# Optimization experiments

Hardware: AMD Instinct MI355X
Metric: run time of the kernel (lower is better)

## Reference

```python
import jax, jax.numpy as jnp
import numpy as np

N = 50000          # nodes
E = 800000         # directed edges (avg degree 16)
IN_F = 1433        # Cora num_features
N_CLS = 7          # Cora num_classes
HEADS = 8
HID = 32
NEG_SLOPE = 0.2    # PyG GATConv default negative_slope


def gat_conv(x, src, dst, W, a_src, a_dst, bias, heads, out_ch):
    """PyG GATConv (concat=True, add_self_loops=True, eval mode)."""
    n = x.shape[0]
    h = (x @ W).reshape(n, heads, out_ch)            # [N, H, C]
    # add self loops (PyG default)
    loop = jnp.arange(n, dtype=src.dtype)
    src = jnp.concatenate([src, loop])
    dst = jnp.concatenate([dst, loop])
    # attention logits per edge: a_src . h_src + a_dst . h_dst
    alpha_src = (h * a_src).sum(-1)                  # [N, H]
    alpha_dst = (h * a_dst).sum(-1)                  # [N, H]
    e = jax.nn.leaky_relu(alpha_src[src] + alpha_dst[dst], NEG_SLOPE)  # [E+N, H]
    # segment softmax over incoming edges of each destination node
    m = jax.ops.segment_max(e, dst, num_segments=n)  # [N, H]
    p = jnp.exp(e - m[dst])
    denom = jax.ops.segment_sum(p, dst, num_segments=n)
    alpha = p / denom[dst]                           # [E+N, H]
    # attention-weighted scatter-aggregate of source features
    out = jax.ops.segment_sum(h[src] * alpha[:, :, None], dst, num_segments=n)  # [N, H, C]
    return out.reshape(n, heads * out_ch) + bias


def setup_inputs() -> dict:
    key = jax.random.key(0)
    ks = jax.random.split(key, 12)
    s = 0.05
    x = jax.random.normal(ks[0], (N, IN_F), dtype=jnp.float32)
    edge_index = jax.random.randint(ks[1], (2, E), 0, N, dtype=jnp.int32)
    W1 = jax.random.normal(ks[2], (IN_F, HEADS * HID), dtype=jnp.float32) * s
    att_src1 = jax.random.normal(ks[3], (HEADS, HID), dtype=jnp.float32) * s
    att_dst1 = jax.random.normal(ks[4], (HEADS, HID), dtype=jnp.float32) * s
    bias1 = jnp.zeros((HEADS * HID,), dtype=jnp.float32)
    W2 = jax.random.normal(ks[5], (HEADS * HID, HEADS * N_CLS), dtype=jnp.float32) * s
    att_src2 = jax.random.normal(ks[6], (HEADS, N_CLS), dtype=jnp.float32) * s
    att_dst2 = jax.random.normal(ks[7], (HEADS, N_CLS), dtype=jnp.float32) * s
    bias2 = jnp.zeros((HEADS * N_CLS,), dtype=jnp.float32)
    return {
        "x": x, "edge_index": edge_index,
        "W1": W1, "att_src1": att_src1, "att_dst1": att_dst1, "bias1": bias1,
        "W2": W2, "att_src2": att_src2, "att_dst2": att_dst2, "bias2": bias2,
    }


def reference(x, edge_index, W1, att_src1, att_dst1, bias1,
              W2, att_src2, att_dst2, bias2):
    src, dst = edge_index[0], edge_index[1]
    # dropout (p=0.6) is identity in eval mode
    h = gat_conv(x, src, dst, W1, att_src1, att_dst1, bias1, HEADS, HID)
    h = jax.nn.elu(h)
    out = gat_conv(h, src, dst, W2, att_src2, att_dst2, bias2, HEADS, N_CLS)
    return out  # [N, HEADS * N_CLS]
```

## Files before the change

### kernel.cpp

```cpp
#include <hip/hip_runtime.h>
#include <math.h>

typedef short s16x8 __attribute__((ext_vector_type(8)));
typedef float f32x4 __attribute__((ext_vector_type(4)));

#define SLOPE 0.2f
#define K1 1433
#define KP 1440
#define NKB 45

static __device__ __forceinline__ float leaky(float x) {
  return x > 0.f ? x : SLOPE * x;
}

static __device__ __forceinline__ unsigned short f2bf(float f) {
  unsigned u = __builtin_bit_cast(unsigned, f);
  u += 0x7FFFu + ((u >> 16) & 1u);
  return (unsigned short)(u >> 16);
}
static __device__ __forceinline__ float bf2f(unsigned short h) {
  unsigned u = ((unsigned)h) << 16;
  return __builtin_bit_cast(float, u);
}

__global__ void w1t_kernel(const float* __restrict__ W1,
                           unsigned short* __restrict__ w1f) {
  int tid = blockIdx.x * 256 + threadIdx.x;
  if (tid >= NKB * 2 * 16 * 64) return;
  int l = tid & 63;
  int chunk = tid >> 6;
  int ntg = chunk & 15;
  int hl = (chunk >> 4) & 1;
  int kb = chunk >> 5;
  int n = ntg * 16 + (l & 15);
  int kbase = kb * 32 + (l >> 4) * 8;
  unsigned short o[8];
#pragma unroll
  for (int e = 0; e < 8; ++e) {
    int k = kbase + e;
    float v = (k < K1) ? W1[(long)k * 256 + n] : 0.f;
    unsigned short h = f2bf(v);
    o[e] = hl ? f2bf(v - bf2f(h)) : h;
  }
  *(ulonglong2*)(w1f + (long)tid * 8) = *(ulonglong2*)o;
}

__global__ __launch_bounds__(256) void gemm1_mfma_kernel(
    const float* __restrict__ A, const unsigned short* __restrict__ w1f,
    float* __restrict__ C, int M) {
  __shared__ unsigned short As[8 * 2 * 64 * 8];
  __shared__ unsigned short Bs[8 * 2 * 64 * 8];
  const int t = threadIdx.x;
  const int w = t >> 6, l = t & 63;
  const int wm = w >> 1, wn = w & 1;
  const int row0 = blockIdx.x * 128;
  const int nblk = blockIdx.y;

  f32x4 acc[4][4];
#pragma unroll
  for (int mt = 0; mt < 4; ++mt)
#pragma unroll
    for (int nt = 0; nt < 4; ++nt)
#pragma unroll
      for (int r = 0; r < 4; ++r) acc[mt][nt][r] = 0.f;

  const int sr = t >> 1;
  const int sk = (t & 1) * 16;
  const int smt = sr >> 4;
  const int slr = sr & 15;

  for (int kb = 0; kb < NKB; ++kb) {
    const int k0 = kb * 32;
#pragma unroll
    for (int q = 0; q < 4; ++q) {
      int c = w * 4 + q;
      int nt = c >> 1, hl = c & 1;
      const unsigned short* gsrc =
          w1f + ((((long)kb * 2 + hl) * 16 + nblk * 8 + nt) * 64 + l) * 8;
      unsigned short* ldst = &Bs[(nt * 2 + hl) * 512];
      __builtin_amdgcn_global_load_lds(
          (const __attribute__((address_space(1))) unsigned int*)gsrc,
          (__attribute__((address_space(3))) unsigned int*)ldst, 16, 0, 0);
    }
    {
      int grow = row0 + sr;
      float v[16];
      if (grow < M) {
        const float* ap = A + (long)grow * K1;
#pragma unroll
        for (int i = 0; i < 16; ++i) {
          int gk = k0 + sk + i;
          v[i] = (gk < K1) ? ap[gk] : 0.f;
        }
      } else {
#pragma unroll
        for (int i = 0; i < 16; ++i) v[i] = 0.f;
      }
#pragma unroll
      for (int g = 0; g < 2; ++g) {
        unsigned short hv[8], lv[8];
#pragma unroll
        for (int e = 0; e < 8; ++e) {
          float f = v[g * 8 + e];
          unsigned short h = f2bf(f);
          hv[e] = h;
          lv[e] = f2bf(f - bf2f(h));
        }
        int lane_dst = slr + 16 * (sk / 8 + g);
        *(ulonglong2*)&As[((smt * 2 + 0) * 64 + lane_dst) * 8] = *(ulonglong2*)hv;
        *(ulonglong2*)&As[((smt * 2 + 1) * 64 + lane_dst) * 8] = *(ulonglong2*)lv;
      }
    }
    __syncthreads();
    {
      s16x8 bh[4], bl[4];
#pragma unroll
      for (int nt = 0; nt < 4; ++nt) {
        int ng = wn * 4 + nt;
        bh[nt] = *(const s16x8*)&Bs[(ng * 2 + 0) * 512 + l * 8];
        bl[nt] = *(const s16x8*)&Bs[(ng * 2 + 1) * 512 + l * 8];
      }
#pragma unroll
      for (int mt = 0; mt < 4; ++mt) {
        int mg = wm * 4 + mt;
        s16x8 ah = *(const s16x8*)&As[(mg * 2 + 0) * 512 + l * 8];
        s16x8 al = *(const s16x8*)&As[(mg * 2 + 1) * 512 + l * 8];
#pragma unroll
        for (int nt = 0; nt < 4; ++nt) {
          acc[mt][nt] = __builtin_amdgcn_mfma_f32_16x16x32_bf16(
              ah, bh[nt], acc[mt][nt], 0, 0, 0);
          acc[mt][nt] = __builtin_amdgcn_mfma_f32_16x16x32_bf16(
              ah, bl[nt], acc[mt][nt], 0, 0, 0);
          acc[mt][nt] = __builtin_amdgcn_mfma_f32_16x16x32_bf16(
              al, bh[nt], acc[mt][nt], 0, 0, 0);
        }
      }
    }
    __syncthreads();
  }
  const int crow4 = (l >> 4) * 4;
  const int ccol = l & 15;
#pragma unroll
  for (int mt = 0; mt < 4; ++mt) {
#pragma unroll
    for (int r = 0; r < 4; ++r) {
      int grow = row0 + wm * 64 + mt * 16 + crow4 + r;
      if (grow < M) {
#pragma unroll
        for (int nt = 0; nt < 4; ++nt) {
          int gcol = nblk * 128 + wn * 64 + nt * 16 + ccol;
          C[(long)grow * 256 + gcol] = acc[mt][nt][r];
        }
      }
    }
  }
}

__global__ void alpha1_kernel(const float* __restrict__ h1,
    const float* __restrict__ a_src, const float* __restrict__ a_dst,
    float* __restrict__ as_o, float* __restrict__ ad_o, int N) {
  int i = blockIdx.x * blockDim.x + threadIdx.x;
  if (i >= N * 8) return;
  int h = i & 7;
  const float* hp = h1 + (long)(i >> 3) * 256 + h * 32;
  const float* sp = a_src + h * 32;
  const float* dp = a_dst + h * 32;
  float s1 = 0.f, s2 = 0.f;
#pragma unroll
  for (int c = 0; c < 32; c += 4) {
    float4 v = *(const float4*)(hp + c);
    float4 ws = *(const float4*)(sp + c);
    float4 wd = *(const float4*)(dp + c);
    s1 += v.x * ws.x + v.y * ws.y + v.z * ws.z + v.w * ws.w;
    s2 += v.x * wd.x + v.y * wd.y + v.z * wd.z + v.w * wd.w;
  }
  as_o[i] = s1;
  ad_o[i] = s2;
}

__global__ void hist_kernel(const int* __restrict__ dst, int* __restrict__ cnt,
                            int E, int N) {
  int e = blockIdx.x * blockDim.x + threadIdx.x;
  if (e >= E + N) return;
  int d = (e < E) ? dst[e] : (e - E);
  atomicAdd(&cnt[d], 1);
}

__global__ __launch_bounds__(1024) void scan_kernel(
    const int* __restrict__ cnt, int* __restrict__ rowptr,
    int* __restrict__ cursor, int N) {
  __shared__ int part[1024];
  const int tid = threadIdx.x;
  const int chunk = (N + 1023) / 1024;
  const int base = tid * chunk;
  const int lim = min(base + chunk, N);
  int sum = 0;
  for (int i = base; i < lim; ++i) sum += cnt[i];
  part[tid] = sum;
  __syncthreads();
  for (int off = 1; off < 1024; off <<= 1) {
    int v = (tid >= off) ? part[tid - off] : 0;
    __syncthreads();
    part[tid] += v;
    __syncthreads();
  }
  int run = (tid == 0) ? 0 : part[tid - 1];
  for (int i = base; i < lim; ++i) {
    rowptr[i] = run;
    cursor[i] = run;
    run += cnt[i];
  }
  if (tid == 1023) rowptr[N] = part[1023];
}

__global__ void scatter_kernel(const int* __restrict__ src,
    const int* __restrict__ dst, int* __restrict__ cursor,
    int* __restrict__ csr_src, int E, int N) {
  int e = blockIdx.x * blockDim.x + threadIdx.x;
  if (e >= E + N) return;
  int s, d;
  if (e < E) { s = src[e]; d = dst[e]; } else { s = e - E; d = s; }
  int pos = atomicAdd(&cursor[d], 1);
  csr_src[pos] = s;
}

__global__ __launch_bounds__(256) void agg1_fused_kernel(
    const int* __restrict__ rowptr, const int* __restrict__ csr_src,
    const float* __restrict__ as_, const float* __restrict__ ad_,
    const float* __restrict__ h1, const float* __restrict__ bias,
    float* __restrict__ act, int N) {
  int d = blockIdx.x * 4 + (threadIdx.x >> 6);
  if (d >= N) return;
  int l = threadIdx.x & 63;
  int h = l >> 3;
  int rs = rowptr[d], re = rowptr[d + 1];
  float adv = ad_[d * 8 + h];
  float4 acc = make_float4(0.f, 0.f, 0.f, 0.f);
  float den = 0.f;
  for (int i = rs; i < re; ++i) {
    int s = csr_src[i];
    float a = __expf(leaky(as_[s * 8 + h] + adv));
    den += a;
    float4 v = *(const float4*)(h1 + (long)s * 256 + l * 4);
    acc.x += a * v.x; acc.y += a * v.y; acc.z += a * v.z; acc.w += a * v.w;
  }
  float inv = 1.f / den;
  float4 b = *(const float4*)(bias + l * 4);
  float4 o;
  o.x = acc.x * inv + b.x; o.y = acc.y * inv + b.y;
  o.z = acc.z * inv + b.z; o.w = acc.w * inv + b.w;
  o.x = o.x > 0.f ? o.x : expm1f(o.x);
  o.y = o.y > 0.f ? o.y : expm1f(o.y);
  o.z = o.z > 0.f ? o.z : expm1f(o.z);
  o.w = o.w > 0.f ? o.w : expm1f(o.w);
  *(float4*)(act + (long)d * 256 + l * 4) = o;
}

__global__ __launch_bounds__(256) void gemm2_kernel(const float* __restrict__ act,
    const float* __restrict__ W2, const float* __restrict__ a_src2,
    const float* __restrict__ a_dst2, float* __restrict__ h2,
    float* __restrict__ as_o, float* __restrict__ ad_o, int N) {
  __shared__ float Ws[256 * 56];
  for (int i = threadIdx.x; i < 256 * 56; i += 256) Ws[i] = W2[i];
  __syncthreads();
  int n = blockIdx.x * 32 + (threadIdx.x >> 3);
  int h = threadIdx.x & 7;
  if (n >= N) return;
  const float* ap = act + (long)n * 256;
  float acc[7] = {0.f, 0.f, 0.f, 0.f, 0.f, 0.f, 0.f};
  for (int k0 = 0; k0 < 256; k0 += 4) {
    float4 a = *(const float4*)(ap + k0);
    float av[4] = {a.x, a.y, a.z, a.w};
#pragma unroll
    for (int kk = 0; kk < 4; ++kk) {
      const float* wp = &Ws[(k0 + kk) * 56 + h * 7];
#pragma unroll
      for (int j = 0; j < 7; ++j) acc[j] += av[kk] * wp[j];
    }
  }
  float* hp = h2 + (long)n * 56 + h * 7;
  float s1 = 0.f, s2 = 0.f;
#pragma unroll
  for (int j = 0; j < 7; ++j) {
    hp[j] = acc[j];
    s1 += acc[j] * a_src2[h * 7 + j];
    s2 += acc[j] * a_dst2[h * 7 + j];
  }
  as_o[n * 8 + h] = s1;
  ad_o[n * 8 + h] = s2;
}

__global__ __launch_bounds__(256) void agg2_fused_kernel(
    const int* __restrict__ rowptr, const int* __restrict__ csr_src,
    const float* __restrict__ as_, const float* __restrict__ ad_,
    const float* __restrict__ h2, const float* __restrict__ bias,
    float* __restrict__ out, int N) {
  int d = blockIdx.x * 4 + (threadIdx.x >> 6);
  if (d >= N) return;
  int l = threadIdx.x & 63;
  int h = l >> 3, j = l & 7;
  int rs = rowptr[d], re = rowptr[d + 1];
  float adv = ad_[d * 8 + h];
  float acc = 0.f, den = 0.f;
  for (int i = rs; i < re; ++i) {
    int s = csr_src[i];
    float a = __expf(leaky(as_[s * 8 + h] + adv));
    den += a;
    if (j < 7) acc += a * h2[(long)s * 56 + h * 7 + j];
  }
  if (j < 7) out[(long)d * 56 + h * 7 + j] = acc / den + bias[h * 7 + j];
}

extern "C" void kernel_launch(void* const* d_in, const int* in_sizes, int n_in,
                              void* d_out, int out_size, void* d_ws, size_t ws_size,
                              hipStream_t stream) {
  const float* x    = (const float*)d_in[0];
  const int*   ei   = (const int*)d_in[1];
  const float* W1   = (const float*)d_in[2];
  const float* asr1 = (const float*)d_in[3];
  const float* adt1 = (const float*)d_in[4];
  const float* b1   = (const float*)d_in[5];
  const float* W2   = (const float*)d_in[6];
  const float* asr2 = (const float*)d_in[7];
  const float* adt2 = (const float*)d_in[8];
  const float* b2   = (const float*)d_in[9];
  float* out = (float*)d_out;

  const int N = in_sizes[0] / K1;
  const int E = in_sizes[1] / 2;
  const int* src = ei;
  const int* dst = ei + E;

  float* ws = (float*)d_ws;
  float* h1  = ws; ws += (long)N * 256;
  float* act = ws; ws += (long)N * 256;
  float* h2  = ws; ws += (long)N * 56;
  float* as1 = ws; ws += N * 8;
  float* ad1 = ws; ws += N * 8;
  float* as2 = ws; ws += N * 8;
  float* ad2 = ws; ws += N * 8;
  unsigned short* w1f = (unsigned short*)ws; ws += NKB * 2 * 16 * 64 * 8 / 2;
  int* cnt     = (int*)ws; ws += N;
  int* rowptr  = (int*)ws; ws += N + 1;
  int* cursor  = (int*)ws; ws += N;
  int* csr_src = (int*)ws; ws += E + N;

  hipMemsetAsync(cnt, 0, (size_t)N * sizeof(int), stream);

  dim3 blk(256);

  hist_kernel<<<dim3((E + N + 255) / 256), blk, 0, stream>>>(dst, cnt, E, N);
  scan_kernel<<<dim3(1), dim3(1024), 0, stream>>>(cnt, rowptr, cursor, N);
  scatter_kernel<<<dim3((E + N + 255) / 256), blk, 0, stream>>>(
      src, dst, cursor, csr_src, E, N);
  {
    int tot = NKB * 2 * 16 * 64;
    w1t_kernel<<<dim3((tot + 255) / 256), blk, 0, stream>>>(W1, w1f);
  }

  gemm1_mfma_kernel<<<dim3((N + 127) / 128, 2), blk, 0, stream>>>(x, w1f, h1, N);
  alpha1_kernel<<<dim3((N * 8 + 255) / 256), blk, 0, stream>>>(h1, asr1, adt1, as1, ad1, N);
  agg1_fused_kernel<<<dim3((N + 3) / 4), blk, 0, stream>>>(
      rowptr, csr_src, as1, ad1, h1, b1, act, N);
  gemm2_kernel<<<dim3((N + 31) / 32), blk, 0, stream>>>(act, W2, asr2, adt2, h2, as2, ad2, N);
  agg2_fused_kernel<<<dim3((N + 3) / 4), blk, 0, stream>>>(
      rowptr, csr_src, as2, ad2, h2, b2, out, N);
}
```

Before: 888.4 us.

## Double-buffer gemm1 LDS tiles and cover full N per 64-row block

Reshapes the first-layer GEMM so each block computes 64 rows across all 256 output columns, replacing 128 rows by 128 columns over a 2-wide grid. The A matrix (x) is therefore read from global memory once instead of twice. The K loop is double-buffered: the next slice of B is loaded asynchronously to LDS and the next A slice is prefetched into registers while MFMAs run on the current buffers, so only one barrier is needed per iteration. The cost is more LDS per block (larger B tile, two buffers), which may lower occupancy, plus a smaller M tile.

```diff
diff --git a/kernel.cpp b/kernel.cpp
--- a/kernel.cpp
+++ b/kernel.cpp
@@ -48,13 +48,11 @@
 __global__ __launch_bounds__(256) void gemm1_mfma_kernel(
     const float* __restrict__ A, const unsigned short* __restrict__ w1f,
     float* __restrict__ C, int M) {
-  __shared__ unsigned short As[8 * 2 * 64 * 8];
-  __shared__ unsigned short Bs[8 * 2 * 64 * 8];
+  __shared__ unsigned short As[2][4 * 2 * 64 * 8];
+  __shared__ unsigned short Bs[2][16 * 2 * 64 * 8];
   const int t = threadIdx.x;
   const int w = t >> 6, l = t & 63;
-  const int wm = w >> 1, wn = w & 1;
-  const int row0 = blockIdx.x * 128;
-  const int nblk = blockIdx.y;
+  const int row0 = blockIdx.x * 64;
 
   f32x4 acc[4][4];
 #pragma unroll
@@ -64,79 +62,101 @@
 #pragma unroll
       for (int r = 0; r < 4; ++r) acc[mt][nt][r] = 0.f;
 
-  const int sr = t >> 1;
-  const int sk = (t & 1) * 16;
-  const int smt = sr >> 4;
-  const int slr = sr & 15;
-
+  const int sr = t >> 2, sg = t & 3;
+  const int smt = sr >> 4, slr = sr & 15;
+  const int lane_dst = slr + 16 * sg;
+  const bool rowok = (row0 + sr) < M;
+  const float* arow = A + (long)(row0 + sr) * K1;
+
+  float v[8];
+
+#pragma unroll
+  for (int q = 0; q < 8; ++q) {
+    int c = w * 8 + q, ng = c >> 1, hl = c & 1;
+    const unsigned short* gsrc = w1f + ((((long)0 * 2 + hl) * 16 + ng) * 64 + l) * 8;
+    unsigned short* ldst = &Bs[0][(ng * 2 + hl) * 512];
+    __builtin_amdgcn_global_load_lds(
+        (const __attribute__((address_space(1))) unsigned int*)gsrc,
+        (__attribute__((address_space(3))) unsigned int*)ldst, 16, 0, 0);
+  }
+  {
+    int kbase = sg * 8;
+#pragma unroll
+    for (int i = 0; i < 8; ++i) {
+      int gk = kbase + i;
+      v[i] = (rowok && gk < K1) ? arow[gk] : 0.f;
+    }
+    unsigned short hv[8], lv[8];
+#pragma unroll
+    for (int e = 0; e < 8; ++e) {
+      unsigned short h = f2bf(v[e]);
+      hv[e] = h;
+      lv[e] = f2bf(v[e] - bf2f(h));
+    }
+    *(ulonglong2*)&As[0][((smt * 2 + 0) * 64 + lane_dst) * 8] = *(ulonglong2*)hv;
+    *(ulonglong2*)&As[0][((smt * 2 + 1) * 64 + lane_dst) * 8] = *(ulonglong2*)lv;
+  }
+  __syncthreads();
+
+  int cur = 0;
   for (int kb = 0; kb < NKB; ++kb) {
-    const int k0 = kb * 32;
-#pragma unroll
-    for (int q = 0; q < 4; ++q) {
-      int c = w * 4 + q;
-      int nt = c >> 1, hl = c & 1;
-      const unsigned short* gsrc =
-          w1f + ((((long)kb * 2 + hl) * 16 + nblk * 8 + nt) * 64 + l) * 8;
-      unsigned short* ldst = &Bs[(nt * 2 + hl) * 512];
-      __builtin_amdgcn_global_load_lds(
-          (const __attribute__((address_space(1))) unsigned int*)gsrc,
-          (__attribute__((address_space(3))) unsigned int*)ldst, 16, 0, 0);
+    const int nxt = kb + 1;
+    if (nxt < NKB) {
+#pragma unroll
+      for (int q = 0; q < 8; ++q) {
+        int c = w * 8 + q, ng = c >> 1, hl = c & 1;
+        const unsigned short* gsrc =
+            w1f + ((((long)nxt * 2 + hl) * 16 + ng) * 64 + l) * 8;
+        unsigned short* ldst = &Bs[cur ^ 1][(ng * 2 + hl) * 512];
+        __builtin_amdgcn_global_load_lds(
+            (const __attribute__((address_space(1))) unsigned int*)gsrc,
+            (__attribute__((address_space(3))) unsigned int*)ldst, 16, 0, 0);
+      }
+      int kbase = nxt * 32 + sg * 8;
+#pragma unroll
+      for (int i = 0; i < 8; ++i) {
+        int gk = kbase + i;
+        v[i] = (rowok && gk < K1) ? arow[gk] : 0.f;
+      }
     }
     {
-      int grow = row0 + sr;
-      float v[16];
-      if (grow < M) {
-        const float* ap = A + (long)grow * K1;
-#pragma unroll
-        for (int i = 0; i < 16; ++i) {
-          int gk = k0 + sk + i;
-          v[i] = (gk < K1) ? ap[gk] : 0.f;
+      s16x8 ah[4], al[4];
+#pragma unroll
+      for (int mt = 0; mt < 4; ++mt) {
+        ah[mt] = *(const s16x8*)&As[cur][(mt * 2 + 0) * 512 + l * 8];
+        al[mt] = *(const s16x8*)&As[cur][(mt * 2 + 1) * 512 + l * 8];
+      }
+#pragma unroll
+      for (int nt = 0; nt < 4; ++nt) {
+        int ng = w * 4 + nt;
+        s16x8 bh = *(const s16x8*)&Bs[cur][(ng * 2 + 0) * 512 + l * 8];
+        s16x8 bl = *(const s16x8*)&Bs[cur][(ng * 2 + 1) * 512 + l * 8];
+#pragma unroll
+        for (int mt = 0; mt < 4; ++mt) {
+          acc[mt][nt] = __builtin_amdgcn_mfma_f32_16x16x32_bf16(
+              ah[mt], bh, acc[mt][nt], 0, 0, 0);
+          acc[mt][nt] = __builtin_amdgcn_mfma_f32_16x16x32_bf16(
+              ah[mt], bl, acc[mt][nt], 0, 0, 0);
+          acc[mt][nt] = __builtin_amdgcn_mfma_f32_16x16x32_bf16(
+              al[mt], bh, acc[mt][nt], 0, 0, 0);
         }
-      } else {
-#pragma unroll
-        for (int i = 0; i < 16; ++i) v[i] = 0.f;
-      }
-#pragma unroll
-      for (int g = 0; g < 2; ++g) {
-        unsigned short hv[8], lv[8];
-#pragma unroll
-        for (int e = 0; e < 8; ++e) {
-          float f = v[g * 8 + e];
-          unsigned short h = f2bf(f);
-          hv[e] = h;
-          lv[e] = f2bf(f - bf2f(h));
-        }
-        int lane_dst = slr + 16 * (sk / 8 + g);
-        *(ulonglong2*)&As[((smt * 2 + 0) * 64 + lane_dst) * 8] = *(ulonglong2*)hv;
-        *(ulonglong2*)&As[((smt * 2 + 1) * 64 + lane_dst) * 8] = *(ulonglong2*)lv;
-      }
-    }
-    __syncthreads();
-    {
-      s16x8 bh[4], bl[4];
-#pragma unroll
-      for (int nt = 0; nt < 4; ++nt) {
-        int ng = wn * 4 + nt;
-        bh[nt] = *(const s16x8*)&Bs[(ng * 2 + 0) * 512 + l * 8];
-        bl[nt] = *(const s16x8*)&Bs[(ng * 2 + 1) * 512 + l * 8];
-      }
-#pragma unroll
-      for (int mt = 0; mt < 4; ++mt) {
-        int mg = wm * 4 + mt;
-        s16x8 ah = *(const s16x8*)&As[(mg * 2 + 0) * 512 + l * 8];
-        s16x8 al = *(const s16x8*)&As[(mg * 2 + 1) * 512 + l * 8];
-#pragma unroll
-        for (int nt = 0; nt < 4; ++nt) {
-          acc[mt][nt] = __builtin_amdgcn_mfma_f32_16x16x32_bf16(
-              ah, bh[nt], acc[mt][nt], 0, 0, 0);
-          acc[mt][nt] = __builtin_amdgcn_mfma_f32_16x16x32_bf16(
-              ah, bl[nt], acc[mt][nt], 0, 0, 0);
-          acc[mt][nt] = __builtin_amdgcn_mfma_f32_16x16x32_bf16(
-              al, bh[nt], acc[mt][nt], 0, 0, 0);
-        }
-      }
-    }
-    __syncthreads();
+      }
+    }
+    if (nxt < NKB) {
+      unsigned short hv[8], lv[8];
+#pragma unroll
+      for (int e = 0; e < 8; ++e) {
+        unsigned short h = f2bf(v[e]);
+        hv[e] = h;
+        lv[e] = f2bf(v[e] - bf2f(h));
+      }
+      *(ulonglong2*)&As[cur ^ 1][((smt * 2 + 0) * 64 + lane_dst) * 8] =
+          *(ulonglong2*)hv;
+      *(ulonglong2*)&As[cur ^ 1][((smt * 2 + 1) * 64 + lane_dst) * 8] =
+          *(ulonglong2*)lv;
+      __syncthreads();
+    }
+    cur ^= 1;
   }
   const int crow4 = (l >> 4) * 4;
   const int ccol = l & 15;
@@ -144,11 +164,11 @@
   for (int mt = 0; mt < 4; ++mt) {
 #pragma unroll
     for (int r = 0; r < 4; ++r) {
-      int grow = row0 + wm * 64 + mt * 16 + crow4 + r;
+      int grow = row0 + mt * 16 + crow4 + r;
       if (grow < M) {
 #pragma unroll
         for (int nt = 0; nt < 4; ++nt) {
-          int gcol = nblk * 128 + wn * 64 + nt * 16 + ccol;
+          int gcol = w * 64 + nt * 16 + ccol;
           C[(long)grow * 256 + gcol] = acc[mt][nt][r];
         }
       }
@@ -358,7 +378,7 @@
     w1t_kernel<<<dim3((tot + 255) / 256), blk, 0, stream>>>(W1, w1f);
   }
 
-  gemm1_mfma_kernel<<<dim3((N + 127) / 128, 2), blk, 0, stream>>>(x, w1f, h1, N);
+  gemm1_mfma_kernel<<<dim3((N + 63) / 64), blk, 0, stream>>>(x, w1f, h1, N);
   alpha1_kernel<<<dim3((N * 8 + 255) / 256), blk, 0, stream>>>(h1, asr1, adt1, as1, ad1, N);
   agg1_fused_kernel<<<dim3((N + 3) / 4), blk, 0, stream>>>(
       rowptr, csr_src, as1, ad1, h1, b1, act, N);
```

After: 742.6 us. -16.4%, faster.
